# Performance work log

Hardware: AMD Instinct MI355X
Metric: run time of the kernel (lower is better)

Reference implementation:

```python
import jax, jax.numpy as jnp
import numpy as np

T, B, A, I, H, L = 256, 64, 512, 1024, 1024, 2
STDV = 1.0 / np.sqrt(H)

def _uniform(key, shape):
    return jax.random.uniform(key, shape, jnp.float32, -STDV, STDV)

def setup_inputs() -> dict:
    key = jax.random.key(0)
    ks = jax.random.split(key, 11)
    return {
        "attention": jax.random.normal(ks[0], (T, B, A), jnp.float32),
        "x": jax.random.normal(ks[1], (T, B, I), jnp.float32),
        "ping": jax.random.normal(ks[2], (B,), jnp.float32),  # unused by module
        "h0": jax.random.normal(ks[3], (L, B, H), jnp.float32),
        "c0": jax.random.normal(ks[4], (L, B, H), jnp.float32),
        "weight_ah": _uniform(ks[5], (L, A, 4 * H)),
        "weight_ih": _uniform(ks[6], (L, I, 4 * H)),  # input_size == hidden_size so layers stack
        "weight_hh": _uniform(ks[7], (L, H, 4 * H)),
        "bias_ah": _uniform(ks[8], (L, 4 * H)),
        "bias_ih": _uniform(ks[9], (L, 4 * H)),
        "bias_hh": _uniform(ks[10], (L, 4 * H)),
    }

def reference(attention, x, ping, h0, c0, weight_ah, weight_ih, weight_hh, bias_ah, bias_ih, bias_hh):
    # Faithful to SACILSTM.forward: only attention[0] is used (fixed across t),
    # ping is unused; per layer l, state is initialized from init_states[l].
    a0 = attention[0]  # [B, A]
    inputs = x  # [T, B, I]
    h_lasts, c_lasts = [], []
    for l in range(h0.shape[0]):
        w_hh = weight_hh[l]
        # Precompute the time-invariant + input-dependent part of the gates.
        const = a0 @ weight_ah[l] + bias_ah[l] + bias_ih[l] + bias_hh[l]  # [B, 4H]
        xg = jnp.einsum('tbi,ij->tbj', inputs, weight_ih[l]) + const  # [T, B, 4H]

        def step(carry, xg_t):
            h, c = carry
            gates = xg_t + h @ w_hh
            i_g, f_g, g_g, o_g = jnp.split(gates, 4, axis=-1)
            c = jax.nn.sigmoid(f_g) * c + jax.nn.sigmoid(i_g) * jnp.tanh(g_g)
            h = jax.nn.sigmoid(o_g) * jnp.tanh(c)
            return (h, c), h

        (h_T, c_T), hs = jax.lax.scan(step, (h0[l], c0[l]), xg)
        inputs = hs  # [T, B, H] feeds next layer
        h_lasts.append(h_T)
        c_lasts.append(c_T)
    # (self.h[:, -1], (self.h[-1], self.c[-1])) flattened
    return hs, jnp.stack(h_lasts), jnp.stack(c_lasts)
```

## Files before the change

kernel.cpp:

```cpp
#include <hip/hip_runtime.h>
#include <hip/hip_bf16.h>
#include <stdint.h>

#define TT 256
#define BH 65536
#define B4H 262144
#define OUT_HL 16777216
#define OUT_CL (16777216 + 131072)
#define NBLK 256
#define SLAB 65536

typedef __attribute__((ext_vector_type(8))) short bf16x8;
typedef __attribute__((ext_vector_type(4))) float f32x4;
typedef __attribute__((ext_vector_type(4))) unsigned int u32x4;
typedef __attribute__((ext_vector_type(2))) unsigned int u32x2;

__device__ __forceinline__ ushort f2bf(float v) {
    union { float f; uint32_t u; } x; x.f = v;
    uint32_t r = x.u + 0x7fff + ((x.u >> 16) & 1);
    return (ushort)(r >> 16);
}
__device__ __forceinline__ float sigf(float x) { return 1.f / (1.f + __expf(-x)); }


__global__ __launch_bounds__(256) void k_prep_wt(const float* __restrict__ wih,
                                                 const float* __restrict__ whh,
                                                 ushort* __restrict__ Wt) {
    __shared__ ushort tile[64][65];
    const int l = blockIdx.z;
    const int k0 = blockIdx.x * 64;
    const int col0 = blockIdx.y * 64;
    const int tid = threadIdx.x;
    const int cl = tid & 63, ks = tid >> 6;
    const float* src;
    int krow0;
    if (k0 < 1024) { src = wih + (size_t)l * 1024 * 4096; krow0 = k0; }
    else           { src = whh + (size_t)l * 1024 * 4096; krow0 = k0 - 1024; }
#pragma unroll
    for (int i = 0; i < 16; ++i) {
        int kl = ks + i * 4;
        tile[kl][cl] = f2bf(src[(size_t)(krow0 + kl) * 4096 + col0 + cl]);
    }
    __syncthreads();
    const int g0 = col0 >> 10, ub = col0 & 1023;
    ushort* dst = Wt + (size_t)l * 4096 * 2048;
    const int klane = tid & 63;
#pragma unroll
    for (int i = 0; i < 16; ++i) {
        int cl2 = (tid >> 6) + i * 4;
        int row = (ub + cl2) * 4 + g0;
        ushort* p = dst + (size_t)row * 2048 + k0 + klane;
        uint v = (uint)tile[klane][cl2];
        asm volatile("global_store_short %0, %1, off sc0 sc1"
                     :: "v"(p), "v"(v) : "memory");
    }
}

__global__ __launch_bounds__(256) void k_cast_x(const float* __restrict__ x,
                                                ushort* __restrict__ xbfF) {
    int i = blockIdx.x * 256 + threadIdx.x;
    int k8 = i & 127, b = (i >> 7) & 63, t = i >> 13;
    const float4* xs = (const float4*)(x + (((size_t)t * 64 + b) * 1024 + k8 * 8));
    float4 a = xs[0], c = xs[1];
    uint4 pk;
    pk.x = (uint)f2bf(a.x) | ((uint)f2bf(a.y) << 16);
    pk.y = (uint)f2bf(a.z) | ((uint)f2bf(a.w) << 16);
    pk.z = (uint)f2bf(c.x) | ((uint)f2bf(c.y) << 16);
    pk.w = (uint)f2bf(c.z) | ((uint)f2bf(c.w) << 16);
    size_t off = (size_t)t * SLAB + (size_t)(b >> 4) * 16384 +
                 (size_t)(k8 >> 2) * 512 + (size_t)(k8 & 3) * 128 + (size_t)(b & 15) * 8;
    *(uint4*)(xbfF + off) = pk;
}

__global__ __launch_bounds__(256) void k_const(const float* __restrict__ attn,
                                               const float* __restrict__ wah,
                                               const float* __restrict__ bah,
                                               const float* __restrict__ bih,
                                               const float* __restrict__ bhh,
                                               float* __restrict__ constg) {
    const int tid = threadIdx.x;
    const int col = blockIdx.x * 256 + tid;
    const int b0 = blockIdx.y * 8;
    const int l = blockIdx.z;
    const float* W = wah + (size_t)l * 512 * 4096;
    float acc[8] = {0.f, 0.f, 0.f, 0.f, 0.f, 0.f, 0.f, 0.f};
    for (int k = 0; k < 512; ++k) {
        float wv = W[(size_t)k * 4096 + col];
#pragma unroll
        for (int j = 0; j < 8; ++j) acc[j] += attn[(b0 + j) * 512 + k] * wv;
    }
    float bias = bah[l * 4096 + col] + bih[l * 4096 + col] + bhh[l * 4096 + col];
    float* cg = constg + (size_t)l * B4H;
#pragma unroll
    for (int j = 0; j < 8; ++j) cg[(size_t)(b0 + j) * 4096 + col] = acc[j] + bias;
}

__global__ __launch_bounds__(256) void k_init(const float* __restrict__ h0,
                                              ushort* __restrict__ hs0F,
                                              ushort* __restrict__ h1s0,
                                              unsigned* __restrict__ flags) {
    int i = blockIdx.x * 256 + threadIdx.x;
    if (i < 16384) {
        int k8 = i & 127, b = (i >> 7) & 63, l = i >> 13;
        const float* src = h0 + ((size_t)(l * 64 + b) * 1024 + k8 * 8);
        uint4 pk;
        pk.x = (uint)f2bf(src[0]) | ((uint)f2bf(src[1]) << 16);
        pk.y = (uint)f2bf(src[2]) | ((uint)f2bf(src[3]) << 16);
        pk.z = (uint)f2bf(src[4]) | ((uint)f2bf(src[5]) << 16);
        pk.w = (uint)f2bf(src[6]) | ((uint)f2bf(src[7]) << 16);
        size_t off = (size_t)(b >> 4) * 16384 + (size_t)(k8 >> 2) * 512 +
                     (size_t)(k8 & 3) * 128 + (size_t)(b & 15) * 8;
        *(uint4*)((l == 0 ? hs0F : h1s0) + off) = pk;
    }
    if (i < NBLK) flags[i] = 0u;
}

#define ISSUE(BUF, BASE)                                                       \
    do { _Pragma("unroll")                                                     \
        for (int _i = 0; _i < 8; ++_i)                                         \
            asm volatile("global_load_dwordx4 %0, %1, off"                     \
                         : "=v"(BUF[_i]) : "v"((BASE) + _i * 512)); } while (0)

#define CHUNK(BUF, KTG0, N, A0, A1)                                            \
    do {                                                                       \
        asm volatile("s_waitcnt vmcnt(" #N ")" ::: "memory");                  \
        __builtin_amdgcn_sched_barrier(0x100);                                 \
        _Pragma("unroll")                                                      \
        for (int _i = 0; _i < 8; ++_i) {                                       \
            int _ktg = (KTG0) + _i;                                            \
            bf16x8 _b0 = *(const bf16x8*)(wlds + (size_t)_ktg * 1024 + lane * 8);       \
            bf16x8 _b1 = *(const bf16x8*)(wlds + (size_t)_ktg * 1024 + 512 + lane * 8); \
            A0 = __builtin_amdgcn_mfma_f32_16x16x32_bf16(BUF[_i], _b0, A0, 0, 0, 0);    \
            A1 = __builtin_amdgcn_mfma_f32_16x16x32_bf16(BUF[_i], _b1, A1, 0, 0, 0);    \
        }                                                                      \
    } while (0)

#define POLL128(FB, TGT)                                                       \
    do {                                                                       \
        const unsigned* _fp = (FB) + lane * 2;                                 \
        while (true) {                                                         \
            u32x2 _f;                                                          \
            asm volatile("global_load_dwordx2 %0, %1, off sc0 sc1\n\t"         \
                         "s_waitcnt vmcnt(0)"                                  \
                         : "=v"(_f) : "v"(_fp) : "memory");                    \
            if (__all(_f.x >= (TGT) && _f.y >= (TGT))) break;                  \
            __builtin_amdgcn_s_sleep(1);                                       \
        }                                                                      \
    } while (0)

__global__ __launch_bounds__(512, 2) void k_persist(
        const ushort* __restrict__ xbfF,
        ushort* __restrict__ hs0F,
        const ushort* __restrict__ h1s0,
        ushort* Wt,
        const float* __restrict__ constg,
        const float* __restrict__ c0,
        float* __restrict__ out,
        unsigned* __restrict__ flags) {
    __shared__ ushort wlds[65536];
    __shared__ float gt[2][4][2][16][18];
    __shared__ unsigned mbx[2];

    const int tid = threadIdx.x;
    const int w = tid >> 6, lane = tid & 63;
    const int kh = w >> 2, m = w & 3;
    const int bid = blockIdx.x;
    const int layer = bid >> 7, ub = bid & 127;
    const int u0g = ub * 8;

    {
        bf16x8 vst[16];
#pragma unroll
        for (int i = 0; i < 16; ++i) {
            int c = i * 512 + tid;
            int lp = c & 63, nt = (c >> 6) & 1, ktg = c >> 7;
            int colp = u0g * 4 + nt * 16 + (lp & 15);
            int kk = ktg * 32 + (lp >> 4) * 8;
            const ushort* src = Wt + ((size_t)(layer * 4096 + colp)) * 2048 + kk;
            asm volatile("global_load_dwordx4 %0, %1, off sc0 sc1"
                         : "=v"(vst[i]) : "v"(src));
        }
        asm volatile("s_waitcnt vmcnt(0)" ::: "memory");
        __builtin_amdgcn_sched_barrier(0);
#pragma unroll
        for (int i = 0; i < 16; ++i) {
            int c = i * 512 + tid;
            *(bf16x8*)(wlds + (size_t)c * 8) = vst[i];
        }
    }
    if (tid == 0) { mbx[0] = 0u; mbx[1] = 0u; }

    const int b_e = (w << 3) | (lane >> 3);
    const int u_off = lane & 7;
    const int u_e = u0g + u_off;
    float cg[4];
#pragma unroll
    for (int g = 0; g < 4; ++g)
        cg[g] = constg[(size_t)layer * B4H + (size_t)b_e * 4096 + g * 1024 + u_e];
    float creg = c0[layer * BH + b_e * 1024 + u_e];
    const int mb = b_e >> 4, blb = b_e & 15, ntb = u_off >> 2, cpb = (u_off & 3) * 4;
    const size_t hoffL = (size_t)mb * 16384 + (size_t)(ub >> 2) * 512 +
                         (size_t)(ub & 3) * 128 + (size_t)blb * 8;

    const size_t fro = (size_t)m * 16384 + (size_t)lane * 8;
    unsigned* f0 = flags;
    unsigned* f1 = flags + 128;

    __syncthreads();

    if (layer == 0) {
        bf16x8 bufXa[8], bufXb[8];
        {
            const ushort* ax = xbfF + fro + kh * 8192;
            ISSUE(bufXa, ax); ISSUE(bufXb, ax + 4096);
            asm volatile("s_waitcnt vmcnt(0)" ::: "memory");
            __builtin_amdgcn_sched_barrier(0);
        }
        for (int s = 0; s < TT; ++s) {
            f32x4 aE0 = {0,0,0,0}, aO0 = {0,0,0,0};
            f32x4 aE1 = {0,0,0,0}, aO1 = {0,0,0,0};
            bf16x8 bufHa[8], bufHb[8];
            CHUNK(bufXa, kh * 16,     0, aE0, aE1);
            CHUNK(bufXb, kh * 16 + 8, 0, aO0, aO1);
            if (s >= 1 && w == 0) POLL128(f0, (unsigned)s);
            __syncthreads();
            {
                const ushort* ah = hs0F + (size_t)s * SLAB + fro + kh * 8192;
                ISSUE(bufHa, ah); ISSUE(bufHb, ah + 4096);
                const ushort* ax = xbfF + (size_t)((s + 1) & 255) * SLAB + fro + kh * 8192;
                ISSUE(bufXa, ax); ISSUE(bufXb, ax + 4096);
                CHUNK(bufHa, 32 + kh * 16,     24, aE0, aE1);
                CHUNK(bufHb, 32 + kh * 16 + 8, 16, aO0, aO1);
            }
            {
                const int cc = lane & 15, r0 = (lane >> 4) * 4;
#pragma unroll
                for (int r = 0; r < 4; ++r) {
                    gt[kh][m][0][r0 + r][cc] = aE0[r] + aO0[r];
                    gt[kh][m][1][r0 + r][cc] = aE1[r] + aO1[r];
                }
            }
            __syncthreads();
            float g4[4];
#pragma unroll
            for (int g = 0; g < 4; ++g)
                g4[g] = gt[0][mb][ntb][blb][cpb + g] + gt[1][mb][ntb][blb][cpb + g] + cg[g];
            float si = sigf(g4[0]), sf = sigf(g4[1]), so = sigf(g4[3]);
            float cn = sf * creg + si * (2.f * sigf(2.f * g4[2]) - 1.f);
            float hv = so * (2.f * sigf(2.f * cn) - 1.f);
            creg = cn;
            uint hb = (uint)f2bf(hv);
            uint p0 = __shfl(hb, (lane & 56) + 0), p1 = __shfl(hb, (lane & 56) + 1);
            uint p2 = __shfl(hb, (lane & 56) + 2), p3 = __shfl(hb, (lane & 56) + 3);
            uint p4 = __shfl(hb, (lane & 56) + 4), p5 = __shfl(hb, (lane & 56) + 5);
            uint p6 = __shfl(hb, (lane & 56) + 6), p7 = __shfl(hb, (lane & 56) + 7);
            u32x4 hp;
            hp.x = (p0 & 0xffffu) | (p1 << 16);
            hp.y = (p2 & 0xffffu) | (p3 << 16);
            hp.z = (p4 & 0xffffu) | (p5 << 16);
            hp.w = (p6 & 0xffffu) | (p7 << 16);
            ushort* hdst = hs0F + (size_t)(s + 1) * SLAB + hoffL;
            if (u_off == 0)
                asm volatile("global_store_dwordx4 %0, %1, off sc0 sc1"
                             :: "v"(hdst), "v"(hp) : "memory");
            asm volatile("s_waitcnt vmcnt(0)" ::: "memory");
            __syncthreads();
            if (tid == 0) {
                unsigned tgt = (unsigned)(s + 1);
                unsigned* fp = f0 + ub;
                asm volatile("global_store_dword %0, %1, off sc0 sc1"
                             :: "v"(fp), "v"(tgt) : "memory");
            }
            if (s == TT - 1) {
                int idx = b_e * 1024 + u_e;
                out[OUT_HL + idx] = hv;
                out[OUT_CL + idx] = cn;
            }
        }
    } else {
        for (int s = 1; s <= TT; ++s) {
            const int t1 = s - 1;
            f32x4 aE0 = {0,0,0,0}, aO0 = {0,0,0,0};
            f32x4 aE1 = {0,0,0,0}, aO1 = {0,0,0,0};
            bf16x8 bufA[8], bufB[8], bufC[8], bufD[8];
            if (w == 0) {
                POLL128(f0, (unsigned)s);
                if (lane == 0)
                    __hip_atomic_store(&mbx[0], (unsigned)s, __ATOMIC_RELEASE,
                                       __HIP_MEMORY_SCOPE_WORKGROUP);
            }
            if (w == 4) {
                if (s >= 2) POLL128(f1, (unsigned)s);
                if (lane == 0)
                    __hip_atomic_store(&mbx[1], (unsigned)s, __ATOMIC_RELEASE,
                                       __HIP_MEMORY_SCOPE_WORKGROUP);
            }
            while (__hip_atomic_load(&mbx[kh], __ATOMIC_ACQUIRE,
                                     __HIP_MEMORY_SCOPE_WORKGROUP) < (unsigned)s)
                __builtin_amdgcn_s_sleep(1);
            {
                const ushort* a = (kh == 0)
                    ? hs0F + (size_t)s * SLAB + fro
                    : (t1 == 0 ? h1s0 + fro
                               : (const ushort*)Wt + (size_t)(t1 - 1) * SLAB + fro);
                ISSUE(bufA, a);
                ISSUE(bufB, a + 4096);
                ISSUE(bufC, a + 8192);
                ISSUE(bufD, a + 12288);
                CHUNK(bufA, kh * 32,      24, aE0, aE1);
                CHUNK(bufB, kh * 32 + 8,  16, aO0, aO1);
                CHUNK(bufC, kh * 32 + 16,  8, aE0, aE1);
                CHUNK(bufD, kh * 32 + 24,  0, aO0, aO1);
            }
            {
                const int cc = lane & 15, r0 = (lane >> 4) * 4;
#pragma unroll
                for (int r = 0; r < 4; ++r) {
                    gt[kh][m][0][r0 + r][cc] = aE0[r] + aO0[r];
                    gt[kh][m][1][r0 + r][cc] = aE1[r] + aO1[r];
                }
            }
            __syncthreads();
            float g4[4];
#pragma unroll
            for (int g = 0; g < 4; ++g)
                g4[g] = gt[0][mb][ntb][blb][cpb + g] + gt[1][mb][ntb][blb][cpb + g] + cg[g];
            float si = sigf(g4[0]), sf = sigf(g4[1]), so = sigf(g4[3]);
            float cn = sf * creg + si * (2.f * sigf(2.f * g4[2]) - 1.f);
            float hv = so * (2.f * sigf(2.f * cn) - 1.f);
            creg = cn;
            uint hb = (uint)f2bf(hv);
            uint p0 = __shfl(hb, (lane & 56) + 0), p1 = __shfl(hb, (lane & 56) + 1);
            uint p2 = __shfl(hb, (lane & 56) + 2), p3 = __shfl(hb, (lane & 56) + 3);
            uint p4 = __shfl(hb, (lane & 56) + 4), p5 = __shfl(hb, (lane & 56) + 5);
            uint p6 = __shfl(hb, (lane & 56) + 6), p7 = __shfl(hb, (lane & 56) + 7);
            u32x4 hp;
            hp.x = (p0 & 0xffffu) | (p1 << 16);
            hp.y = (p2 & 0xffffu) | (p3 << 16);
            hp.z = (p4 & 0xffffu) | (p5 << 16);
            hp.w = (p6 & 0xffffu) | (p7 << 16);
            ushort* hdst = Wt + (size_t)t1 * SLAB + hoffL;
            if (u_off == 0)
                asm volatile("global_store_dwordx4 %0, %1, off sc0 sc1"
                             :: "v"(hdst), "v"(hp) : "memory");
            asm volatile("s_waitcnt vmcnt(0)" ::: "memory");
            __syncthreads();
            if (tid == 0) {
                unsigned tgt = (unsigned)(s + 1);
                unsigned* fp = f1 + ub;
                asm volatile("global_store_dword %0, %1, off sc0 sc1"
                             :: "v"(fp), "v"(tgt) : "memory");
            }
            {
                float o0 = __shfl(hv, (lane & 56) + 0), o1 = __shfl(hv, (lane & 56) + 1);
                float o2 = __shfl(hv, (lane & 56) + 2), o3 = __shfl(hv, (lane & 56) + 3);
                float o4 = __shfl(hv, (lane & 56) + 4), o5 = __shfl(hv, (lane & 56) + 5);
                float o6 = __shfl(hv, (lane & 56) + 6), o7 = __shfl(hv, (lane & 56) + 7);
                if (u_off == 0) {
                    float* op = out + (size_t)t1 * BH + (size_t)b_e * 1024 + u0g;
                    float4 v0 = {o0, o1, o2, o3}, v1 = {o4, o5, o6, o7};
                    *(float4*)op = v0;
                    *(float4*)(op + 4) = v1;
                }
                if (t1 == TT - 1) {
                    int idx = b_e * 1024 + u_e;
                    out[OUT_HL + BH + idx] = hv;
                    out[OUT_CL + BH + idx] = cn;
                }
            }
        }
    }
}

extern "C" void kernel_launch(void* const* d_in, const int* in_sizes, int n_in,
                              void* d_out, int out_size, void* d_ws, size_t ws_size,
                              hipStream_t stream) {
    const float* attn = (const float*)d_in[0];
    const float* x    = (const float*)d_in[1];
    const float* h0   = (const float*)d_in[3];
    const float* c0   = (const float*)d_in[4];
    const float* wah  = (const float*)d_in[5];
    const float* wih  = (const float*)d_in[6];
    const float* whh  = (const float*)d_in[7];
    const float* bah  = (const float*)d_in[8];
    const float* bih  = (const float*)d_in[9];
    const float* bhh  = (const float*)d_in[10];
    float* out = (float*)d_out;

    char* ws = (char*)d_ws;
    ushort*   Wt     = (ushort*)(ws);
    ushort*   xbfF   = (ushort*)(ws + 33554432);
    ushort*   hs0F   = (ushort*)(ws + 67108864);
    ushort*   h1s0   = (ushort*)(ws + 100794368);
    float*    constg = (float*)(ws + 100925440);
    unsigned* flags  = (unsigned*)(ws + 103022592);

    hipLaunchKernelGGL(k_prep_wt, dim3(32, 64, 2), dim3(256), 0, stream, wih, whh, Wt);
    hipLaunchKernelGGL(k_cast_x, dim3(8192), dim3(256), 0, stream, x, xbfF);
    hipLaunchKernelGGL(k_const, dim3(16, 8, 2), dim3(256), 0, stream, attn, wah, bah, bih, bhh, constg);
    hipLaunchKernelGGL(k_init, dim3(64), dim3(256), 0, stream, h0, hs0F, h1s0, flags);

    void* args[] = { (void*)&xbfF, (void*)&hs0F, (void*)&h1s0, (void*)&Wt,
                     (void*)&constg, (void*)&c0, (void*)&out, (void*)&flags };
    hipLaunchCooperativeKernel((void*)k_persist, dim3(NBLK), dim3(512), args, 0, stream);
}
```

Baseline: 1.572 ms.

## Replace block barriers with mailbox spins and split layer-1 K work across both halves

In layer 0, the per-step __syncthreads after polling is replaced by an LDS mailbox spin. The x-chunk MFMAs are now issued after the h loads start, with the next x loads deferred until those MFMAs finish. In layer 1, each kh half now does half of both the input-h contribution and the recurrent-h contribution, instead of one half owning each source. Every wave therefore waits on the layer-0 flag first and the layer-1 flag second. This lets the input-side work overlap the wait on the recurrent dependency and halves register buffering, at the cost of extra flag waits for all waves and a changed reduction split.

```diff
diff --git a/kernel.cpp b/kernel.cpp
--- a/kernel.cpp
+++ b/kernel.cpp
@@ -148,6 +148,14 @@
         }                                                                      \
     } while (0)
 
+#define MBX_SET(I, V)                                                          \
+    __hip_atomic_store(&mbx[I], (unsigned)(V), __ATOMIC_RELEASE,               \
+                       __HIP_MEMORY_SCOPE_WORKGROUP)
+#define MBX_SPIN(I, V)                                                         \
+    while (__hip_atomic_load(&mbx[I], __ATOMIC_ACQUIRE,                        \
+                             __HIP_MEMORY_SCOPE_WORKGROUP) < (unsigned)(V))    \
+        __builtin_amdgcn_s_sleep(1)
+
 __global__ __launch_bounds__(512, 2) void k_persist(
         const ushort* __restrict__ xbfF,
         ushort* __restrict__ hs0F,
@@ -202,7 +210,7 @@
     const size_t hoffL = (size_t)mb * 16384 + (size_t)(ub >> 2) * 512 +
                          (size_t)(ub & 3) * 128 + (size_t)blb * 8;
 
-    const size_t fro = (size_t)m * 16384 + (size_t)lane * 8;
+    const size_t froq = (size_t)m * 16384 + (size_t)kh * 8192 + (size_t)lane * 8;
     unsigned* f0 = flags;
     unsigned* f1 = flags + 128;
 
@@ -211,7 +219,7 @@
     if (layer == 0) {
         bf16x8 bufXa[8], bufXb[8];
         {
-            const ushort* ax = xbfF + fro + kh * 8192;
+            const ushort* ax = xbfF + froq;
             ISSUE(bufXa, ax); ISSUE(bufXb, ax + 4096);
             asm volatile("s_waitcnt vmcnt(0)" ::: "memory");
             __builtin_amdgcn_sched_barrier(0);
@@ -220,18 +228,19 @@
             f32x4 aE0 = {0,0,0,0}, aO0 = {0,0,0,0};
             f32x4 aE1 = {0,0,0,0}, aO1 = {0,0,0,0};
             bf16x8 bufHa[8], bufHb[8];
-            CHUNK(bufXa, kh * 16,     0, aE0, aE1);
-            CHUNK(bufXb, kh * 16 + 8, 0, aO0, aO1);
-            if (s >= 1 && w == 0) POLL128(f0, (unsigned)s);
-            __syncthreads();
-            {
-                const ushort* ah = hs0F + (size_t)s * SLAB + fro + kh * 8192;
-                ISSUE(bufHa, ah); ISSUE(bufHb, ah + 4096);
-                const ushort* ax = xbfF + (size_t)((s + 1) & 255) * SLAB + fro + kh * 8192;
-                ISSUE(bufXa, ax); ISSUE(bufXb, ax + 4096);
-                CHUNK(bufHa, 32 + kh * 16,     24, aE0, aE1);
-                CHUNK(bufHb, 32 + kh * 16 + 8, 16, aO0, aO1);
-            }
+            if (w == 0) {
+                if (s >= 1) POLL128(f0, (unsigned)s);
+                if (lane == 0) MBX_SET(0, s);
+            }
+            MBX_SPIN(0, s);
+            const ushort* ah = hs0F + (size_t)s * SLAB + froq;
+            ISSUE(bufHa, ah); ISSUE(bufHb, ah + 4096);
+            const ushort* ax = xbfF + (size_t)((s + 1) & 255) * SLAB + froq;
+            CHUNK(bufXa, kh * 16,     32, aE0, aE1);
+            CHUNK(bufXb, kh * 16 + 8, 32, aO0, aO1);
+            ISSUE(bufXa, ax); ISSUE(bufXb, ax + 4096);
+            CHUNK(bufHa, 32 + kh * 16,     24, aE0, aE1);
+            CHUNK(bufHb, 32 + kh * 16 + 8, 16, aO0, aO1);
             {
                 const int cc = lane & 15, r0 = (lane >> 4) * 4;
 #pragma unroll
@@ -282,36 +291,26 @@
             const int t1 = s - 1;
             f32x4 aE0 = {0,0,0,0}, aO0 = {0,0,0,0};
             f32x4 aE1 = {0,0,0,0}, aO1 = {0,0,0,0};
-            bf16x8 bufA[8], bufB[8], bufC[8], bufD[8];
+            bf16x8 bufA[8], bufB[8];
             if (w == 0) {
                 POLL128(f0, (unsigned)s);
-                if (lane == 0)
-                    __hip_atomic_store(&mbx[0], (unsigned)s, __ATOMIC_RELEASE,
-                                       __HIP_MEMORY_SCOPE_WORKGROUP);
-            }
+                if (lane == 0) MBX_SET(0, s);
+            }
+            MBX_SPIN(0, s);
+            const ushort* aih = hs0F + (size_t)s * SLAB + froq;
+            ISSUE(bufA, aih); ISSUE(bufB, aih + 4096);
             if (w == 4) {
                 if (s >= 2) POLL128(f1, (unsigned)s);
-                if (lane == 0)
-                    __hip_atomic_store(&mbx[1], (unsigned)s, __ATOMIC_RELEASE,
-                                       __HIP_MEMORY_SCOPE_WORKGROUP);
-            }
-            while (__hip_atomic_load(&mbx[kh], __ATOMIC_ACQUIRE,
-                                     __HIP_MEMORY_SCOPE_WORKGROUP) < (unsigned)s)
-                __builtin_amdgcn_s_sleep(1);
-            {
-                const ushort* a = (kh == 0)
-                    ? hs0F + (size_t)s * SLAB + fro
-                    : (t1 == 0 ? h1s0 + fro
-                               : (const ushort*)Wt + (size_t)(t1 - 1) * SLAB + fro);
-                ISSUE(bufA, a);
-                ISSUE(bufB, a + 4096);
-                ISSUE(bufC, a + 8192);
-                ISSUE(bufD, a + 12288);
-                CHUNK(bufA, kh * 32,      24, aE0, aE1);
-                CHUNK(bufB, kh * 32 + 8,  16, aO0, aO1);
-                CHUNK(bufC, kh * 32 + 16,  8, aE0, aE1);
-                CHUNK(bufD, kh * 32 + 24,  0, aO0, aO1);
-            }
+                if (lane == 0) MBX_SET(1, s);
+            }
+            CHUNK(bufA, kh * 16,     8, aE0, aE1);
+            CHUNK(bufB, kh * 16 + 8, 0, aO0, aO1);
+            MBX_SPIN(1, s);
+            const ushort* ahh = (t1 == 0 ? h1s0
+                                : (const ushort*)Wt + (size_t)(t1 - 1) * SLAB) + froq;
+            ISSUE(bufA, ahh); ISSUE(bufB, ahh + 4096);
+            CHUNK(bufA, 32 + kh * 16,     8, aE0, aE1);
+            CHUNK(bufB, 32 + kh * 16 + 8, 0, aO0, aO1);
             {
                 const int cc = lane & 15, r0 = (lane >> 4) * 4;
 #pragma unroll
```

Measured after the change: 2.033 ms. 1.29x slower.
